# Kernel optimization log

Hardware: AMD Instinct MI355X
Metric: run time of the kernel (lower is better)

Reference implementation:

```python
import jax, jax.numpy as jnp
import numpy as np

D_MODEL = 512
H = 8
DK = D_MODEL // H  # 64


def setup_inputs() -> dict:
    key = jax.random.key(0)
    ks = jax.random.split(key, 8)
    B, S = 2, 4096
    q = jax.random.normal(ks[0], (B, S, D_MODEL), dtype=jnp.float32)
    k = jax.random.normal(ks[1], (B, S, D_MODEL), dtype=jnp.float32)
    v = jax.random.normal(ks[2], (B, S, D_MODEL), dtype=jnp.float32)
    # per-head projection weights, torch nn.Linear layout [out, in], stacked over heads
    scale = 1.0 / np.sqrt(D_MODEL)
    Wq = jax.random.uniform(ks[3], (H, DK, D_MODEL), jnp.float32, -scale, scale)
    Wk = jax.random.uniform(ks[4], (H, DK, D_MODEL), jnp.float32, -scale, scale)
    Wv = jax.random.uniform(ks[5], (H, DK, D_MODEL), jnp.float32, -scale, scale)
    Wo = jax.random.uniform(ks[6], (D_MODEL, D_MODEL), jnp.float32, -scale, scale)
    # causal mask (True = keep), matches masked_fill(mask.logical_not(), -inf)
    mask = jnp.tril(jnp.ones((S, S), dtype=jnp.bool_))
    return {"q": q, "k": k, "v": v, "Wq": Wq, "Wk": Wk, "Wv": Wv, "Wo": Wo, "mask": mask}


def reference(q, k, v, Wq, Wk, Wv, Wo, mask):
    # per-head projections (stacked): x @ W^T for each head -> [B, H, S, DK]
    qh = jnp.einsum('bsd,hed->bhse', q, Wq)
    kh = jnp.einsum('bsd,hed->bhse', k, Wk)
    vh = jnp.einsum('bsd,hed->bhse', v, Wv)
    scaling = 1.0 / np.sqrt(DK)
    scores = jnp.einsum('bhse,bhte->bhst', qh, kh) * scaling  # [B,H,S,S]
    scores = jnp.where(mask, scores, -jnp.inf)
    attn = jax.nn.softmax(scores, axis=-1)
    heads = jnp.einsum('bhst,bhte->bhse', attn, vh)  # [B,H,S,DK]
    B, _, S, _ = heads.shape
    concat = jnp.transpose(heads, (0, 2, 1, 3)).reshape(B, S, D_MODEL)
    return concat @ Wo.T
```

## Files before the change

kernel.cpp:

```cpp
#include <hip/hip_runtime.h>
#include <hip/hip_bf16.h>
#include <math.h>

typedef __bf16 bf16_t;
typedef __bf16 bf16x8 __attribute__((ext_vector_type(8)));
typedef __bf16 bf16x4 __attribute__((ext_vector_type(4)));
typedef short short4v __attribute__((ext_vector_type(4)));
typedef float f32x4 __attribute__((ext_vector_type(4)));

__device__ __forceinline__ f32x4 mfma_k32(bf16x8 a, bf16x8 b, f32x4 c) {
    return __builtin_amdgcn_mfma_f32_16x16x32_bf16(a, b, c, 0, 0, 0);
}

__device__ __forceinline__ f32x4 mfma_k16(bf16x4 a, bf16x4 b, f32x4 c) {
#if __has_builtin(__builtin_amdgcn_mfma_f32_16x16x16_bf16)
    return __builtin_amdgcn_mfma_f32_16x16x16_bf16(a, b, c, 0, 0, 0);
#elif __has_builtin(__builtin_amdgcn_mfma_f32_16x16x16bf16_1k)
    short4v as, bs;
    __builtin_memcpy(&as, &a, 8);
    __builtin_memcpy(&bs, &b, 8);
    return __builtin_amdgcn_mfma_f32_16x16x16bf16_1k(as, bs, c, 0, 0, 0);
#else
    f32x4 d = c;
    asm volatile("v_mfma_f32_16x16x16_bf16 %0, %1, %2, %0" : "+v"(d) : "v"(a), "v"(b));
    return d;
#endif
}

__device__ __forceinline__ void async16(const bf16_t* g, __bf16* l) {
    __builtin_amdgcn_global_load_lds(
        (const __attribute__((address_space(1))) void*)g,
        (__attribute__((address_space(3))) void*)l, 16, 0, 0);
}

__device__ __forceinline__ int swz_col(int col, int row) {
    return (col & ~63) | ((((col >> 3) & 7) ^ (row & 7)) << 3) | (col & 7);
}

__global__ __launch_bounds__(256) void cvt_x(const float* __restrict__ q,
                                             const float* __restrict__ k,
                                             const float* __restrict__ v,
                                             bf16_t* __restrict__ qc,
                                             bf16_t* __restrict__ kc,
                                             bf16_t* __restrict__ vc) {
    size_t i = ((size_t)blockIdx.x * 256 + threadIdx.x) * 8;
    int row = (int)(i >> 9), col = (int)(i & 511);
    size_t di = (size_t)row * 512 + swz_col(col, row);
    float4 a0 = *(const float4*)(q + i), a1 = *(const float4*)(q + i + 4);
    float4 b0 = *(const float4*)(k + i), b1 = *(const float4*)(k + i + 4);
    float4 c0 = *(const float4*)(v + i), c1 = *(const float4*)(v + i + 4);
    bf16x8 qo, ko, vo;
    qo[0]=(__bf16)a0.x; qo[1]=(__bf16)a0.y; qo[2]=(__bf16)a0.z; qo[3]=(__bf16)a0.w;
    qo[4]=(__bf16)a1.x; qo[5]=(__bf16)a1.y; qo[6]=(__bf16)a1.z; qo[7]=(__bf16)a1.w;
    ko[0]=(__bf16)b0.x; ko[1]=(__bf16)b0.y; ko[2]=(__bf16)b0.z; ko[3]=(__bf16)b0.w;
    ko[4]=(__bf16)b1.x; ko[5]=(__bf16)b1.y; ko[6]=(__bf16)b1.z; ko[7]=(__bf16)b1.w;
    vo[0]=(__bf16)c0.x; vo[1]=(__bf16)c0.y; vo[2]=(__bf16)c0.z; vo[3]=(__bf16)c0.w;
    vo[4]=(__bf16)c1.x; vo[5]=(__bf16)c1.y; vo[6]=(__bf16)c1.z; vo[7]=(__bf16)c1.w;
    *(bf16x8*)(qc + di) = qo;
    *(bf16x8*)(kc + di) = ko;
    *(bf16x8*)(vc + di) = vo;
}

__global__ __launch_bounds__(256) void cvt_w(const float* __restrict__ Wq,
                                             const float* __restrict__ Wk,
                                             const float* __restrict__ Wv,
                                             const float* __restrict__ Wo,
                                             bf16_t* __restrict__ Wc) {
    const int m = blockIdx.y;
    const float* src = m == 0 ? Wq : m == 1 ? Wk : m == 2 ? Wv : Wo;
    const float sc = (m == 0) ? 0.125f * 1.44269504088896f : 1.0f;
    size_t i = ((size_t)blockIdx.x * 256 + threadIdx.x) * 8;
    int row = (int)(i >> 9), col = (int)(i & 511);
    float4 a0 = *(const float4*)(src + i), a1 = *(const float4*)(src + i + 4);
    bf16x8 o;
    o[0]=(__bf16)(a0.x*sc); o[1]=(__bf16)(a0.y*sc); o[2]=(__bf16)(a0.z*sc); o[3]=(__bf16)(a0.w*sc);
    o[4]=(__bf16)(a1.x*sc); o[5]=(__bf16)(a1.y*sc); o[6]=(__bf16)(a1.z*sc); o[7]=(__bf16)(a1.w*sc);
    *(bf16x8*)(Wc + (size_t)m * 262144 + (size_t)row * 512 + swz_col(col, row)) = o;
}

__global__ __launch_bounds__(256) void proj_fused(const bf16_t* __restrict__ xs,
                                                  const bf16_t* __restrict__ Wc,
                                                  bf16_t* __restrict__ qh,
                                                  bf16_t* __restrict__ kh,
                                                  bf16_t* __restrict__ vh) {
    __shared__ __bf16 Asm[64 * 64];
    __shared__ __bf16 Bsm[128 * 64];
    const int z    = blockIdx.z;
    const bf16_t* A = xs + (size_t)z * 4194304;
    const bf16_t* B = Wc + (size_t)z * 262144;
    const int tid  = threadIdx.x;
    const int wave = tid >> 6;
    const int lane = tid & 63;
    const int quad = lane >> 4;
    const int l16  = lane & 15;
    const int swz  = l16 & 7;
    const int m0 = blockIdx.x * 64;
    const int n0 = blockIdx.y * 128;
    const int r8 = lane >> 3;
    const int c8 = (lane & 7) * 8;

    f32x4 acc[8];
    for (int i = 0; i < 8; ++i) acc[i] = (f32x4){0.f, 0.f, 0.f, 0.f};

    for (int kt = 0; kt < 512; kt += 64) {
        __syncthreads();
        for (int j = 0; j < 2; ++j)
            async16(A + (size_t)(m0 + wave * 16 + j * 8 + r8) * 512 + kt + c8,
                    &Asm[(wave * 16 + j * 8) * 64]);
        for (int j = 0; j < 4; ++j)
            async16(B + (size_t)(n0 + wave * 32 + j * 8 + r8) * 512 + kt + c8,
                    &Bsm[(wave * 32 + j * 8) * 64]);
        __syncthreads();

        for (int ks = 0; ks < 2; ++ks) {
            bf16x8 afr = *(const bf16x8*)&Asm[(wave * 16 + l16) * 64 + ((ks * 4 + quad) ^ swz) * 8];
            for (int nt = 0; nt < 8; ++nt) {
                bf16x8 bfr = *(const bf16x8*)&Bsm[(nt * 16 + l16) * 64 + ((ks * 4 + quad) ^ swz) * 8];
                acc[nt] = mfma_k32(afr, bfr, acc[nt]);
            }
        }
    }

    if (z < 2) {
        bf16_t* out = z ? kh : qh;
        for (int nt = 0; nt < 8; ++nt) {
            int e = n0 + nt * 16 + l16;
            int h = e >> 6, el = e & 63;
            for (int r = 0; r < 4; ++r) {
                int row = m0 + wave * 16 + quad * 4 + r;
                int b = row >> 12, s = row & 4095;
                int elp = (((el >> 3) ^ (row & 7)) << 3) | (el & 7);
                out[(((size_t)(b * 8 + h)) * 4096 + s) * 64 + elp] = (bf16_t)acc[nt][r];
            }
        }
    } else {
        const int bb = m0 >> 12;
        const int sbase = m0 & 4095;
        const int chunk = 2 * quad + (wave >> 1);
        const int elo   = 4 * (wave & 1);
        for (int nt = 0; nt < 8; ++nt) {
            int e_g = n0 + nt * 16 + l16;
            int h = e_g >> 6, el = e_g & 63;
            int col = sbase + ((chunk ^ (e_g & 7)) << 3) + elo;
            bf16x4 pk;
            pk[0] = (bf16_t)acc[nt][0]; pk[1] = (bf16_t)acc[nt][1];
            pk[2] = (bf16_t)acc[nt][2]; pk[3] = (bf16_t)acc[nt][3];
            *(bf16x4*)&vh[(((size_t)(bb * 8 + h)) * 64 + el) * 4096 + col] = pk;
        }
    }
}

__global__ __launch_bounds__(256) void gemm_final(const bf16_t* __restrict__ A,
                                                  const bf16_t* __restrict__ B,
                                                  float* __restrict__ out) {
    __shared__ __bf16 Asm[64 * 64];
    __shared__ __bf16 Bsm[128 * 64];
    const int tid  = threadIdx.x;
    const int wave = tid >> 6;
    const int lane = tid & 63;
    const int quad = lane >> 4;
    const int l16  = lane & 15;
    const int swz  = l16 & 7;
    const int m0 = blockIdx.x * 64;
    const int n0 = blockIdx.y * 128;
    const int r8 = lane >> 3;
    const int c8 = (lane & 7) * 8;

    f32x4 acc[8];
    for (int i = 0; i < 8; ++i) acc[i] = (f32x4){0.f, 0.f, 0.f, 0.f};

    for (int kt = 0; kt < 512; kt += 64) {
        __syncthreads();
        for (int j = 0; j < 2; ++j)
            async16(A + (size_t)(m0 + wave * 16 + j * 8 + r8) * 512 + kt + c8,
                    &Asm[(wave * 16 + j * 8) * 64]);
        for (int j = 0; j < 4; ++j)
            async16(B + (size_t)(n0 + wave * 32 + j * 8 + r8) * 512 + kt + c8,
                    &Bsm[(wave * 32 + j * 8) * 64]);
        __syncthreads();

        for (int ks = 0; ks < 2; ++ks) {
            bf16x8 afr = *(const bf16x8*)&Asm[(wave * 16 + l16) * 64 + ((ks * 4 + quad) ^ swz) * 8];
            for (int nt = 0; nt < 8; ++nt) {
                bf16x8 bfr = *(const bf16x8*)&Bsm[(nt * 16 + l16) * 64 + ((ks * 4 + quad) ^ swz) * 8];
                acc[nt] = mfma_k32(afr, bfr, acc[nt]);
            }
        }
    }

    for (int nt = 0; nt < 8; ++nt) {
        int n = n0 + nt * 16 + l16;
        for (int r = 0; r < 4; ++r) {
            int row = m0 + wave * 16 + quad * 4 + r;
            out[(size_t)row * 512 + n] = acc[nt][r];
        }
    }
}

__global__ __launch_bounds__(256) void attn_kernel(const bf16_t* __restrict__ qh,
                                                   const bf16_t* __restrict__ kh,
                                                   const bf16_t* __restrict__ vh,
                                                   bf16_t* __restrict__ ao) {
    __shared__ __bf16 Ksm[2][64 * 64];
    __shared__ __bf16 VTsm[2][64 * 64];
    const int tid  = threadIdx.x;
    const int wave = tid >> 6;
    const int g2   = wave >> 1;
    const int wl   = wave & 1;
    const int lane = tid & 63;
    const int quad = lane >> 4;
    const int l16  = lane & 15;
    const int swz  = l16 & 7;
    const int bh   = blockIdx.y;
    const size_t base = (size_t)bh * 4096 * 64;
    const int r8 = lane >> 3;
    const int c8 = (lane & 7) * 8;
    const int b = bh >> 3, h = bh & 7;

    float* Osc = (float*)&Ksm[0][0];
    float* Lsc = (float*)&VTsm[0][0];

    for (int leg = 0; leg < 2; ++leg) {
        const int qt = leg ? (63 - (int)blockIdx.x) : (int)blockIdx.x;
        const int q0 = qt * 64;

        bf16x8 qf[2][2];
        for (int g = 0; g < 2; ++g) {
            const bf16_t* qp = qh + base + (size_t)(q0 + wl * 32 + g * 16 + l16) * 64;
            qf[g][0] = *(const bf16x8*)(qp + ((quad ^ swz) * 8));
            qf[g][1] = *(const bf16x8*)(qp + (((4 + quad) ^ swz) * 8));
        }

        f32x4 o[2][4];
        for (int g = 0; g < 2; ++g)
            for (int i = 0; i < 4; ++i) o[g][i] = (f32x4){0.f, 0.f, 0.f, 0.f};
        float lsum[2] = {0.f, 0.f};

        const int iters = (qt + 2) >> 1;
        for (int it = 0; it < iters; ++it) {
            const int j0 = it * 128;
            __syncthreads();
            for (int p = 0; p < 2; ++p)
                for (int j = 0; j < 2; ++j) {
                    int row = wave * 16 + j * 8 + r8;
                    async16(kh + base + (size_t)(j0 + p * 64 + row) * 64 + c8,
                            &Ksm[p][(wave * 16 + j * 8) * 64]);
                    async16(vh + (size_t)(bh * 64 + row) * 4096 + j0 + p * 64 + c8,
                            &VTsm[p][(wave * 16 + j * 8) * 64]);
                }
            __syncthreads();

            const int pp = g2;
            const int koff = j0 + pp * 64 - q0;

            f32x4 st[2][4];
            for (int nt = 0; nt < 4; ++nt) {
                bf16x8 kf0 = *(const bf16x8*)&Ksm[pp][(nt * 16 + l16) * 64 + ((quad ^ swz) * 8)];
                bf16x8 kf1 = *(const bf16x8*)&Ksm[pp][(nt * 16 + l16) * 64 + (((4 + quad) ^ swz) * 8)];
                for (int g = 0; g < 2; ++g) {
                    f32x4 z = (f32x4){0.f, 0.f, 0.f, 0.f};
                    z = mfma_k32(kf0, qf[g][0], z);
                    z = mfma_k32(kf1, qf[g][1], z);
                    st[g][nt] = z;
                }
            }

            bf16x4 pf[2][4];
            for (int g = 0; g < 2; ++g) {
                const int qrow = wl * 32 + g * 16 + l16;
                if (koff >= 0) {
                    for (int nt = 0; nt < 4; ++nt)
                        for (int r = 0; r < 4; ++r) {
                            int key = nt * 16 + quad * 4 + r;
                            float p = (key + koff <= qrow) ? exp2f(st[g][nt][r]) : 0.f;
                            lsum[g] += p;
                            pf[g][nt][r] = (bf16_t)p;
                        }
                } else {
                    for (int nt = 0; nt < 4; ++nt)
                        for (int r = 0; r < 4; ++r) {
                            float p = exp2f(st[g][nt][r]);
                            lsum[g] += p;
                            pf[g][nt][r] = (bf16_t)p;
                        }
                }
            }

            for (int dt = 0; dt < 4; ++dt)
                for (int kt2 = 0; kt2 < 2; ++kt2) {
                    bf16x8 vf = *(const bf16x8*)&VTsm[pp][(dt * 16 + l16) * 64 + (((2 * quad + kt2) ^ swz) * 8)];
                    bf16x4 vlo = {vf[0], vf[1], vf[2], vf[3]};
                    bf16x4 vhi = {vf[4], vf[5], vf[6], vf[7]};
                    for (int g = 0; g < 2; ++g) {
                        o[g][dt] = mfma_k16(pf[g][2 * kt2], vlo, o[g][dt]);
                        o[g][dt] = mfma_k16(pf[g][2 * kt2 + 1], vhi, o[g][dt]);
                    }
                }
        }

        __syncthreads();
        if (g2 == 1) {
            for (int g = 0; g < 2; ++g) {
                float ls = lsum[g];
                ls += __shfl_xor(ls, 16);
                ls += __shfl_xor(ls, 32);
                int qb = wl * 32 + g * 16;
                Lsc[qb + l16] = ls;
                for (int dt = 0; dt < 4; ++dt)
                    for (int r = 0; r < 4; ++r)
                        Osc[(qb + quad * 4 + r) * 64 + dt * 16 + l16] = o[g][dt][r];
            }
        }
        __syncthreads();
        if (g2 == 0) {
            for (int g = 0; g < 2; ++g) {
                float ls = lsum[g];
                ls += __shfl_xor(ls, 16);
                ls += __shfl_xor(ls, 32);
                int qb = wl * 32 + g * 16;
                ls += Lsc[qb + l16];
                float linv[4];
                for (int r = 0; r < 4; ++r) linv[r] = 1.0f / __shfl(ls, quad * 4 + r);
                for (int r = 0; r < 4; ++r) {
                    int s_g = q0 + qb + quad * 4 + r;
                    size_t rowoff = ((size_t)(b * 4096 + s_g)) * 512;
                    for (int dt = 0; dt < 4; ++dt) {
                        float ov = o[g][dt][r] + Osc[(qb + quad * 4 + r) * 64 + dt * 16 + l16];
                        int el = dt * 16 + l16;
                        int elp = (((el >> 3) ^ (s_g & 7)) << 3) | (el & 7);
                        ao[rowoff + h * 64 + elp] = (bf16_t)(ov * linv[r]);
                    }
                }
            }
        }
    }
}

extern "C" void kernel_launch(void* const* d_in, const int* in_sizes, int n_in,
                              void* d_out, int out_size, void* d_ws, size_t ws_size,
                              hipStream_t stream) {
    const float* q  = (const float*)d_in[0];
    const float* k  = (const float*)d_in[1];
    const float* v  = (const float*)d_in[2];
    const float* Wq = (const float*)d_in[3];
    const float* Wk = (const float*)d_in[4];
    const float* Wv = (const float*)d_in[5];
    const float* Wo = (const float*)d_in[6];
    float* out = (float*)d_out;

    bf16_t* ws = (bf16_t*)d_ws;
    const size_t R = (size_t)8192 * 512;
    bf16_t* qc = ws;
    bf16_t* kc = ws + R;
    bf16_t* vc = ws + 2 * R;
    bf16_t* vh = ws + 3 * R;
    bf16_t* Wc = ws + 4 * R;
    bf16_t* qh = (bf16_t*)d_out;
    bf16_t* kh = (bf16_t*)d_out + R;
    bf16_t* ao = qc;

    dim3 bb(256);
    cvt_x<<<dim3(2048), bb, 0, stream>>>(q, k, v, qc, kc, vc);
    cvt_w<<<dim3(128, 4), bb, 0, stream>>>(Wq, Wk, Wv, Wo, Wc);
    proj_fused<<<dim3(128, 4, 3), bb, 0, stream>>>(ws, Wc, qh, kh, vh);
    attn_kernel<<<dim3(32, 16), bb, 0, stream>>>(qh, kh, vh, ao);
    gemm_final<<<dim3(128, 4), bb, 0, stream>>>(ao, Wc + 3 * 262144, out);
}
```

Measured before the change: 261.1 us.

## Merge conversion kernels, retile GEMMs to full-N, widen attention to 8 waves

Merges the two fp32-to-bf16 conversion kernels into one launch. The projection and output GEMMs are retiled from 64x128 to 16x512 tiles, with the whole weight slab staged in LDS. The attention kernel moves to 512 threads that process four 64-key blocks per iteration, skips loads and compute for fully masked blocks, and uses a hardware exp2 intrinsic. The cross-wave reduction now combines four partial results. The intent is to cut launch overhead and masked-tile work and to add parallelism, at the cost of more LDS per block, redundant weight loads per tile, and lower GEMM arithmetic intensity.

```diff
diff --git a/kernel.cpp b/kernel.cpp
--- a/kernel.cpp
+++ b/kernel.cpp
@@ -27,6 +27,16 @@
 #endif
 }
 
+__device__ __forceinline__ float fast_exp2(float x) {
+#if __has_builtin(__builtin_amdgcn_exp2f)
+    return __builtin_amdgcn_exp2f(x);
+#else
+    float r;
+    asm("v_exp_f32 %0, %1" : "=v"(r) : "v"(x));
+    return r;
+#endif
+}
+
 __device__ __forceinline__ void async16(const bf16_t* g, __bf16* l) {
     __builtin_amdgcn_global_load_lds(
         (const __attribute__((address_space(1))) void*)g,
@@ -37,45 +47,48 @@
     return (col & ~63) | ((((col >> 3) & 7) ^ (row & 7)) << 3) | (col & 7);
 }
 
-__global__ __launch_bounds__(256) void cvt_x(const float* __restrict__ q,
-                                             const float* __restrict__ k,
-                                             const float* __restrict__ v,
-                                             bf16_t* __restrict__ qc,
-                                             bf16_t* __restrict__ kc,
-                                             bf16_t* __restrict__ vc) {
-    size_t i = ((size_t)blockIdx.x * 256 + threadIdx.x) * 8;
-    int row = (int)(i >> 9), col = (int)(i & 511);
-    size_t di = (size_t)row * 512 + swz_col(col, row);
-    float4 a0 = *(const float4*)(q + i), a1 = *(const float4*)(q + i + 4);
-    float4 b0 = *(const float4*)(k + i), b1 = *(const float4*)(k + i + 4);
-    float4 c0 = *(const float4*)(v + i), c1 = *(const float4*)(v + i + 4);
-    bf16x8 qo, ko, vo;
-    qo[0]=(__bf16)a0.x; qo[1]=(__bf16)a0.y; qo[2]=(__bf16)a0.z; qo[3]=(__bf16)a0.w;
-    qo[4]=(__bf16)a1.x; qo[5]=(__bf16)a1.y; qo[6]=(__bf16)a1.z; qo[7]=(__bf16)a1.w;
-    ko[0]=(__bf16)b0.x; ko[1]=(__bf16)b0.y; ko[2]=(__bf16)b0.z; ko[3]=(__bf16)b0.w;
-    ko[4]=(__bf16)b1.x; ko[5]=(__bf16)b1.y; ko[6]=(__bf16)b1.z; ko[7]=(__bf16)b1.w;
-    vo[0]=(__bf16)c0.x; vo[1]=(__bf16)c0.y; vo[2]=(__bf16)c0.z; vo[3]=(__bf16)c0.w;
-    vo[4]=(__bf16)c1.x; vo[5]=(__bf16)c1.y; vo[6]=(__bf16)c1.z; vo[7]=(__bf16)c1.w;
-    *(bf16x8*)(qc + di) = qo;
-    *(bf16x8*)(kc + di) = ko;
-    *(bf16x8*)(vc + di) = vo;
-}
-
-__global__ __launch_bounds__(256) void cvt_w(const float* __restrict__ Wq,
-                                             const float* __restrict__ Wk,
-                                             const float* __restrict__ Wv,
-                                             const float* __restrict__ Wo,
-                                             bf16_t* __restrict__ Wc) {
-    const int m = blockIdx.y;
-    const float* src = m == 0 ? Wq : m == 1 ? Wk : m == 2 ? Wv : Wo;
-    const float sc = (m == 0) ? 0.125f * 1.44269504088896f : 1.0f;
-    size_t i = ((size_t)blockIdx.x * 256 + threadIdx.x) * 8;
-    int row = (int)(i >> 9), col = (int)(i & 511);
-    float4 a0 = *(const float4*)(src + i), a1 = *(const float4*)(src + i + 4);
-    bf16x8 o;
-    o[0]=(__bf16)(a0.x*sc); o[1]=(__bf16)(a0.y*sc); o[2]=(__bf16)(a0.z*sc); o[3]=(__bf16)(a0.w*sc);
-    o[4]=(__bf16)(a1.x*sc); o[5]=(__bf16)(a1.y*sc); o[6]=(__bf16)(a1.z*sc); o[7]=(__bf16)(a1.w*sc);
-    *(bf16x8*)(Wc + (size_t)m * 262144 + (size_t)row * 512 + swz_col(col, row)) = o;
+__global__ __launch_bounds__(256) void cvt_all(const float* __restrict__ q,
+                                               const float* __restrict__ k,
+                                               const float* __restrict__ v,
+                                               const float* __restrict__ Wq,
+                                               const float* __restrict__ Wk,
+                                               const float* __restrict__ Wv,
+                                               const float* __restrict__ Wo,
+                                               bf16_t* __restrict__ qc,
+                                               bf16_t* __restrict__ kc,
+                                               bf16_t* __restrict__ vc,
+                                               bf16_t* __restrict__ Wc) {
+    const int bx = blockIdx.x;
+    if (bx < 2048) {
+        size_t i = ((size_t)bx * 256 + threadIdx.x) * 8;
+        int row = (int)(i >> 9), col = (int)(i & 511);
+        size_t di = (size_t)row * 512 + swz_col(col, row);
+        float4 a0 = *(const float4*)(q + i), a1 = *(const float4*)(q + i + 4);
+        float4 b0 = *(const float4*)(k + i), b1 = *(const float4*)(k + i + 4);
+        float4 c0 = *(const float4*)(v + i), c1 = *(const float4*)(v + i + 4);
+        bf16x8 qo, ko, vo;
+        qo[0]=(__bf16)a0.x; qo[1]=(__bf16)a0.y; qo[2]=(__bf16)a0.z; qo[3]=(__bf16)a0.w;
+        qo[4]=(__bf16)a1.x; qo[5]=(__bf16)a1.y; qo[6]=(__bf16)a1.z; qo[7]=(__bf16)a1.w;
+        ko[0]=(__bf16)b0.x; ko[1]=(__bf16)b0.y; ko[2]=(__bf16)b0.z; ko[3]=(__bf16)b0.w;
+        ko[4]=(__bf16)b1.x; ko[5]=(__bf16)b1.y; ko[6]=(__bf16)b1.z; ko[7]=(__bf16)b1.w;
+        vo[0]=(__bf16)c0.x; vo[1]=(__bf16)c0.y; vo[2]=(__bf16)c0.z; vo[3]=(__bf16)c0.w;
+        vo[4]=(__bf16)c1.x; vo[5]=(__bf16)c1.y; vo[6]=(__bf16)c1.z; vo[7]=(__bf16)c1.w;
+        *(bf16x8*)(qc + di) = qo;
+        *(bf16x8*)(kc + di) = ko;
+        *(bf16x8*)(vc + di) = vo;
+    } else {
+        const int b2 = bx - 2048;
+        const int m = b2 >> 7;
+        const float* src = m == 0 ? Wq : m == 1 ? Wk : m == 2 ? Wv : Wo;
+        const float sc = (m == 0) ? 0.125f * 1.44269504088896f : 1.0f;
+        size_t i = ((size_t)(b2 & 127) * 256 + threadIdx.x) * 8;
+        int row = (int)(i >> 9), col = (int)(i & 511);
+        float4 a0 = *(const float4*)(src + i), a1 = *(const float4*)(src + i + 4);
+        bf16x8 o;
+        o[0]=(__bf16)(a0.x*sc); o[1]=(__bf16)(a0.y*sc); o[2]=(__bf16)(a0.z*sc); o[3]=(__bf16)(a0.w*sc);
+        o[4]=(__bf16)(a1.x*sc); o[5]=(__bf16)(a1.y*sc); o[6]=(__bf16)(a1.z*sc); o[7]=(__bf16)(a1.w*sc);
+        *(bf16x8*)(Wc + (size_t)m * 262144 + (size_t)row * 512 + swz_col(col, row)) = o;
+    }
 }
 
 __global__ __launch_bounds__(256) void proj_fused(const bf16_t* __restrict__ xs,
@@ -83,8 +96,8 @@
                                                   bf16_t* __restrict__ qh,
                                                   bf16_t* __restrict__ kh,
                                                   bf16_t* __restrict__ vh) {
-    __shared__ __bf16 Asm[64 * 64];
-    __shared__ __bf16 Bsm[128 * 64];
+    __shared__ __bf16 Asm[16 * 64];
+    __shared__ __bf16 Bsm[512 * 64];
     const int z    = blockIdx.z;
     const bf16_t* A = xs + (size_t)z * 4194304;
     const bf16_t* B = Wc + (size_t)z * 262144;
@@ -94,8 +107,7 @@
     const int quad = lane >> 4;
     const int l16  = lane & 15;
     const int swz  = l16 & 7;
-    const int m0 = blockIdx.x * 64;
-    const int n0 = blockIdx.y * 128;
+    const int m0 = blockIdx.x * 16;
     const int r8 = lane >> 3;
     const int c8 = (lane & 7) * 8;
 
@@ -104,18 +116,17 @@
 
     for (int kt = 0; kt < 512; kt += 64) {
         __syncthreads();
-        for (int j = 0; j < 2; ++j)
-            async16(A + (size_t)(m0 + wave * 16 + j * 8 + r8) * 512 + kt + c8,
-                    &Asm[(wave * 16 + j * 8) * 64]);
-        for (int j = 0; j < 4; ++j)
-            async16(B + (size_t)(n0 + wave * 32 + j * 8 + r8) * 512 + kt + c8,
-                    &Bsm[(wave * 32 + j * 8) * 64]);
+        if (wave < 2)
+            async16(A + (size_t)(m0 + wave * 8 + r8) * 512 + kt + c8, &Asm[wave * 8 * 64]);
+        for (int j = 0; j < 16; ++j)
+            async16(B + (size_t)(wave * 128 + j * 8 + r8) * 512 + kt + c8,
+                    &Bsm[(wave * 128 + j * 8) * 64]);
         __syncthreads();
 
         for (int ks = 0; ks < 2; ++ks) {
-            bf16x8 afr = *(const bf16x8*)&Asm[(wave * 16 + l16) * 64 + ((ks * 4 + quad) ^ swz) * 8];
+            bf16x8 afr = *(const bf16x8*)&Asm[l16 * 64 + ((ks * 4 + quad) ^ swz) * 8];
             for (int nt = 0; nt < 8; ++nt) {
-                bf16x8 bfr = *(const bf16x8*)&Bsm[(nt * 16 + l16) * 64 + ((ks * 4 + quad) ^ swz) * 8];
+                bf16x8 bfr = *(const bf16x8*)&Bsm[(wave * 128 + nt * 16 + l16) * 64 + ((ks * 4 + quad) ^ swz) * 8];
                 acc[nt] = mfma_k32(afr, bfr, acc[nt]);
             }
         }
@@ -124,10 +135,10 @@
     if (z < 2) {
         bf16_t* out = z ? kh : qh;
         for (int nt = 0; nt < 8; ++nt) {
-            int e = n0 + nt * 16 + l16;
+            int e = wave * 128 + nt * 16 + l16;
             int h = e >> 6, el = e & 63;
             for (int r = 0; r < 4; ++r) {
-                int row = m0 + wave * 16 + quad * 4 + r;
+                int row = m0 + quad * 4 + r;
                 int b = row >> 12, s = row & 4095;
                 int elp = (((el >> 3) ^ (row & 7)) << 3) | (el & 7);
                 out[(((size_t)(b * 8 + h)) * 4096 + s) * 64 + elp] = (bf16_t)acc[nt][r];
@@ -135,13 +146,14 @@
         }
     } else {
         const int bb = m0 >> 12;
-        const int sbase = m0 & 4095;
-        const int chunk = 2 * quad + (wave >> 1);
-        const int elo   = 4 * (wave & 1);
+        const int sbase = (m0 & 4095) & ~63;
+        const int s5 = (m0 >> 5) & 1;
+        const int mf4 = ((m0 >> 4) & 1) * 4;
+        const int chunk = 2 * quad + s5;
         for (int nt = 0; nt < 8; ++nt) {
-            int e_g = n0 + nt * 16 + l16;
+            int e_g = wave * 128 + nt * 16 + l16;
             int h = e_g >> 6, el = e_g & 63;
-            int col = sbase + ((chunk ^ (e_g & 7)) << 3) + elo;
+            int col = sbase + ((chunk ^ (e_g & 7)) << 3) + mf4;
             bf16x4 pk;
             pk[0] = (bf16_t)acc[nt][0]; pk[1] = (bf16_t)acc[nt][1];
             pk[2] = (bf16_t)acc[nt][2]; pk[3] = (bf16_t)acc[nt][3];
@@ -153,16 +165,15 @@
 __global__ __launch_bounds__(256) void gemm_final(const bf16_t* __restrict__ A,
                                                   const bf16_t* __restrict__ B,
                                                   float* __restrict__ out) {
-    __shared__ __bf16 Asm[64 * 64];
-    __shared__ __bf16 Bsm[128 * 64];
+    __shared__ __bf16 Asm[16 * 64];
+    __shared__ __bf16 Bsm[512 * 64];
     const int tid  = threadIdx.x;
     const int wave = tid >> 6;
     const int lane = tid & 63;
     const int quad = lane >> 4;
     const int l16  = lane & 15;
     const int swz  = l16 & 7;
-    const int m0 = blockIdx.x * 64;
-    const int n0 = blockIdx.y * 128;
+    const int m0 = blockIdx.x * 16;
     const int r8 = lane >> 3;
     const int c8 = (lane & 7) * 8;
 
@@ -171,41 +182,42 @@
 
     for (int kt = 0; kt < 512; kt += 64) {
         __syncthreads();
-        for (int j = 0; j < 2; ++j)
-            async16(A + (size_t)(m0 + wave * 16 + j * 8 + r8) * 512 + kt + c8,
-                    &Asm[(wave * 16 + j * 8) * 64]);
-        for (int j = 0; j < 4; ++j)
-            async16(B + (size_t)(n0 + wave * 32 + j * 8 + r8) * 512 + kt + c8,
-                    &Bsm[(wave * 32 + j * 8) * 64]);
+        if (wave < 2)
+            async16(A + (size_t)(m0 + wave * 8 + r8) * 512 + kt + c8, &Asm[wave * 8 * 64]);
+        for (int j = 0; j < 16; ++j)
+            async16(B + (size_t)(wave * 128 + j * 8 + r8) * 512 + kt + c8,
+                    &Bsm[(wave * 128 + j * 8) * 64]);
         __syncthreads();
 
         for (int ks = 0; ks < 2; ++ks) {
-            bf16x8 afr = *(const bf16x8*)&Asm[(wave * 16 + l16) * 64 + ((ks * 4 + quad) ^ swz) * 8];
+            bf16x8 afr = *(const bf16x8*)&Asm[l16 * 64 + ((ks * 4 + quad) ^ swz) * 8];
             for (int nt = 0; nt < 8; ++nt) {
-                bf16x8 bfr = *(const bf16x8*)&Bsm[(nt * 16 + l16) * 64 + ((ks * 4 + quad) ^ swz) * 8];
+                bf16x8 bfr = *(const bf16x8*)&Bsm[(wave * 128 + nt * 16 + l16) * 64 + ((ks * 4 + quad) ^ swz) * 8];
                 acc[nt] = mfma_k32(afr, bfr, acc[nt]);
             }
         }
     }
 
     for (int nt = 0; nt < 8; ++nt) {
-        int n = n0 + nt * 16 + l16;
-        for (int r = 0; r < 4; ++r) {
-            int row = m0 + wave * 16 + quad * 4 + r;
-            out[(size_t)row * 512 + n] = acc[nt][r];
-        }
-    }
-}
-
-__global__ __launch_bounds__(256) void attn_kernel(const bf16_t* __restrict__ qh,
-                                                   const bf16_t* __restrict__ kh,
-                                                   const bf16_t* __restrict__ vh,
-                                                   bf16_t* __restrict__ ao) {
-    __shared__ __bf16 Ksm[2][64 * 64];
-    __shared__ __bf16 VTsm[2][64 * 64];
+        int n = wave * 128 + nt * 16 + l16;
+        for (int r = 0; r < 4; ++r)
+            out[(size_t)(m0 + quad * 4 + r) * 512 + n] = acc[nt][r];
+    }
+}
+
+__global__ __launch_bounds__(512, 4) void attn_kernel(const bf16_t* __restrict__ qh,
+                                                      const bf16_t* __restrict__ kh,
+                                                      const bf16_t* __restrict__ vh,
+                                                      bf16_t* __restrict__ ao) {
+    __shared__ __bf16 SM[32768];
+    __bf16* KSM = &SM[0];
+    __bf16* VSM = &SM[16384];
+    float* Osc = (float*)SM;
+    float* Lsc = (float*)&SM[24576];
+
     const int tid  = threadIdx.x;
     const int wave = tid >> 6;
-    const int g2   = wave >> 1;
+    const int pp   = wave >> 1;
     const int wl   = wave & 1;
     const int lane = tid & 63;
     const int quad = lane >> 4;
@@ -217,9 +229,6 @@
     const int c8 = (lane & 7) * 8;
     const int b = bh >> 3, h = bh & 7;
 
-    float* Osc = (float*)&Ksm[0][0];
-    float* Lsc = (float*)&VTsm[0][0];
-
     for (int leg = 0; leg < 2; ++leg) {
         const int qt = leg ? (63 - (int)blockIdx.x) : (int)blockIdx.x;
         const int q0 = qt * 64;
@@ -236,50 +245,52 @@
             for (int i = 0; i < 4; ++i) o[g][i] = (f32x4){0.f, 0.f, 0.f, 0.f};
         float lsum[2] = {0.f, 0.f};
 
-        const int iters = (qt + 2) >> 1;
+        const int iters = (qt + 4) >> 2;
         for (int it = 0; it < iters; ++it) {
-            const int j0 = it * 128;
+            const int j0 = it * 256;
+            const int koff = j0 + pp * 64 - q0;
             __syncthreads();
-            for (int p = 0; p < 2; ++p)
-                for (int j = 0; j < 2; ++j) {
-                    int row = wave * 16 + j * 8 + r8;
-                    async16(kh + base + (size_t)(j0 + p * 64 + row) * 64 + c8,
-                            &Ksm[p][(wave * 16 + j * 8) * 64]);
-                    async16(vh + (size_t)(bh * 64 + row) * 4096 + j0 + p * 64 + c8,
-                            &VTsm[p][(wave * 16 + j * 8) * 64]);
-                }
+            if (koff <= 63) {
+                for (int j = 0; j < 4; ++j) {
+                    int row = wl * 32 + j * 8 + r8;
+                    async16(kh + base + (size_t)(j0 + pp * 64 + row) * 64 + c8,
+                            KSM + (pp * 64 + wl * 32 + j * 8) * 64);
+                    async16(vh + (size_t)(bh * 64 + row) * 4096 + j0 + pp * 64 + c8,
+                            VSM + (pp * 64 + wl * 32 + j * 8) * 64);
+                }
+            }
             __syncthreads();
-
-            const int pp = g2;
-            const int koff = j0 + pp * 64 - q0;
+            if (koff > wl * 32 + 31) continue;
 
             f32x4 st[2][4];
             for (int nt = 0; nt < 4; ++nt) {
-                bf16x8 kf0 = *(const bf16x8*)&Ksm[pp][(nt * 16 + l16) * 64 + ((quad ^ swz) * 8)];
-                bf16x8 kf1 = *(const bf16x8*)&Ksm[pp][(nt * 16 + l16) * 64 + (((4 + quad) ^ swz) * 8)];
+                const __bf16* kr = KSM + (pp * 64 + nt * 16 + l16) * 64;
+                bf16x8 kf0 = *(const bf16x8*)(kr + ((quad ^ swz) * 8));
+                bf16x8 kf1 = *(const bf16x8*)(kr + (((4 + quad) ^ swz) * 8));
                 for (int g = 0; g < 2; ++g) {
-                    f32x4 z = (f32x4){0.f, 0.f, 0.f, 0.f};
-                    z = mfma_k32(kf0, qf[g][0], z);
-                    z = mfma_k32(kf1, qf[g][1], z);
-                    st[g][nt] = z;
+                    f32x4 zz = (f32x4){0.f, 0.f, 0.f, 0.f};
+                    zz = mfma_k32(kf0, qf[g][0], zz);
+                    zz = mfma_k32(kf1, qf[g][1], zz);
+                    st[g][nt] = zz;
                 }
             }
 
             bf16x4 pf[2][4];
             for (int g = 0; g < 2; ++g) {
-                const int qrow = wl * 32 + g * 16 + l16;
-                if (koff >= 0) {
+                const int qb = wl * 32 + g * 16;
+                if (koff + 63 <= qb) {
                     for (int nt = 0; nt < 4; ++nt)
                         for (int r = 0; r < 4; ++r) {
-                            int key = nt * 16 + quad * 4 + r;
-                            float p = (key + koff <= qrow) ? exp2f(st[g][nt][r]) : 0.f;
+                            float p = fast_exp2(st[g][nt][r]);
                             lsum[g] += p;
                             pf[g][nt][r] = (bf16_t)p;
                         }
                 } else {
+                    const int qrow = qb + l16;
                     for (int nt = 0; nt < 4; ++nt)
                         for (int r = 0; r < 4; ++r) {
-                            float p = exp2f(st[g][nt][r]);
+                            int key = nt * 16 + quad * 4 + r;
+                            float p = (key + koff <= qrow) ? fast_exp2(st[g][nt][r]) : 0.f;
                             lsum[g] += p;
                             pf[g][nt][r] = (bf16_t)p;
                         }
@@ -288,7 +299,7 @@
 
             for (int dt = 0; dt < 4; ++dt)
                 for (int kt2 = 0; kt2 < 2; ++kt2) {
-                    bf16x8 vf = *(const bf16x8*)&VTsm[pp][(dt * 16 + l16) * 64 + (((2 * quad + kt2) ^ swz) * 8)];
+                    bf16x8 vf = *(const bf16x8*)&VSM[(pp * 64 + dt * 16 + l16) * 64 + (((2 * quad + kt2) ^ swz) * 8)];
                     bf16x4 vlo = {vf[0], vf[1], vf[2], vf[3]};
                     bf16x4 vhi = {vf[4], vf[5], vf[6], vf[7]};
                     for (int g = 0; g < 2; ++g) {
@@ -299,12 +310,13 @@
         }
 
         __syncthreads();
-        if (g2 == 1) {
+        if (pp != 0) {
+            const int pi = pp - 1;
             for (int g = 0; g < 2; ++g) {
                 float ls = lsum[g];
                 ls += __shfl_xor(ls, 16);
                 ls += __shfl_xor(ls, 32);
-                int qb = wl * 32 + g * 16;
+                const int qb = (pi * 2 + wl) * 32 + g * 16;
                 Lsc[qb + l16] = ls;
                 for (int dt = 0; dt < 4; ++dt)
                     for (int r = 0; r < 4; ++r)
@@ -312,20 +324,23 @@
             }
         }
         __syncthreads();
-        if (g2 == 0) {
+        if (pp == 0) {
             for (int g = 0; g < 2; ++g) {
                 float ls = lsum[g];
                 ls += __shfl_xor(ls, 16);
                 ls += __shfl_xor(ls, 32);
-                int qb = wl * 32 + g * 16;
-                ls += Lsc[qb + l16];
+                const int qb = wl * 32 + g * 16;
+                for (int pi = 0; pi < 3; ++pi)
+                    ls += Lsc[(pi * 2 + wl) * 32 + g * 16 + l16];
                 float linv[4];
                 for (int r = 0; r < 4; ++r) linv[r] = 1.0f / __shfl(ls, quad * 4 + r);
                 for (int r = 0; r < 4; ++r) {
                     int s_g = q0 + qb + quad * 4 + r;
                     size_t rowoff = ((size_t)(b * 4096 + s_g)) * 512;
                     for (int dt = 0; dt < 4; ++dt) {
-                        float ov = o[g][dt][r] + Osc[(qb + quad * 4 + r) * 64 + dt * 16 + l16];
+                        float ov = o[g][dt][r];
+                        for (int pi = 0; pi < 3; ++pi)
+                            ov += Osc[((pi * 2 + wl) * 32 + g * 16 + quad * 4 + r) * 64 + dt * 16 + l16];
                         int el = dt * 16 + l16;
                         int elp = (((el >> 3) ^ (s_g & 7)) << 3) | (el & 7);
                         ao[rowoff + h * 64 + elp] = (bf16_t)(ov * linv[r]);
@@ -359,10 +374,8 @@
     bf16_t* kh = (bf16_t*)d_out + R;
     bf16_t* ao = qc;
 
-    dim3 bb(256);
-    cvt_x<<<dim3(2048), bb, 0, stream>>>(q, k, v, qc, kc, vc);
-    cvt_w<<<dim3(128, 4), bb, 0, stream>>>(Wq, Wk, Wv, Wo, Wc);
-    proj_fused<<<dim3(128, 4, 3), bb, 0, stream>>>(ws, Wc, qh, kh, vh);
-    attn_kernel<<<dim3(32, 16), bb, 0, stream>>>(qh, kh, vh, ao);
-    gemm_final<<<dim3(128, 4), bb, 0, stream>>>(ao, Wc + 3 * 262144, out);
-}
+    cvt_all<<<dim3(2560), dim3(256), 0, stream>>>(q, k, v, Wq, Wk, Wv, Wo, qc, kc, vc, Wc);
+    proj_fused<<<dim3(512, 1, 3), dim3(256), 0, stream>>>(ws, Wc, qh, kh, vh);
+    attn_kernel<<<dim3(32, 16), dim3(512), 0, stream>>>(qh, kh, vh, ao);
+    gemm_final<<<dim3(512), dim3(256), 0, stream>>>(ao, Wc + 3 * 262144, out);
+}
```

Result: slower. 285.8 us (+9.5%).
